# Optimization experiments

Hardware: AMD Instinct MI355X
Metric: run time of the kernel (lower is better)

## Reference

```python
import jax, jax.numpy as jnp
import numpy as np

R, TR = 47, 2  # response_size, treat_size


def _lstm_cell(x, h, c, Wih, Whh, bih, bhh):
    # PyTorch gate order: i, f, g, o
    gates = x @ Wih.T + h @ Whh.T + bih + bhh
    i, f, g, o = jnp.split(gates, 4, axis=-1)
    c_new = jax.nn.sigmoid(f) * c + jax.nn.sigmoid(i) * jnp.tanh(g)
    h_new = jax.nn.sigmoid(o) * jnp.tanh(c_new)
    return h_new, c_new


def setup_inputs() -> dict:
    key = jax.random.key(0)
    B, T = 256, 2048
    ks = jax.random.split(key, 20)

    def u(k, shape, H):
        s = 1.0 / np.sqrt(H).astype(np.float32)
        return jax.random.uniform(k, shape, jnp.float32, -s, s)

    return {
        "x_r": jax.random.normal(ks[0], (B, T, R), jnp.float32),
        "x_t": jax.random.normal(ks[1], (B, T, TR), jnp.float32),
        # r_rnn: 2-layer LSTM, input 49 -> hidden 47
        "r_Wih0": u(ks[2], (4 * R, R + TR), R), "r_Whh0": u(ks[3], (4 * R, R), R),
        "r_bih0": u(ks[4], (4 * R,), R), "r_bhh0": u(ks[5], (4 * R,), R),
        "r_Wih1": u(ks[6], (4 * R, R), R), "r_Whh1": u(ks[7], (4 * R, R), R),
        "r_bih1": u(ks[8], (4 * R,), R), "r_bhh1": u(ks[9], (4 * R,), R),
        # t_rnn: 2-layer LSTM, input 96 -> hidden 2
        "t_Wih0": u(ks[10], (4 * TR, 2 * R + TR), TR), "t_Whh0": u(ks[11], (4 * TR, TR), TR),
        "t_bih0": u(ks[12], (4 * TR,), TR), "t_bhh0": u(ks[13], (4 * TR,), TR),
        "t_Wih1": u(ks[14], (4 * TR, TR), TR), "t_Whh1": u(ks[15], (4 * TR, TR), TR),
        "t_bih1": u(ks[16], (4 * TR,), TR), "t_bhh1": u(ks[17], (4 * TR,), TR),
    }


def reference(x_r, x_t,
              r_Wih0, r_Whh0, r_bih0, r_bhh0, r_Wih1, r_Whh1, r_bih1, r_bhh1,
              t_Wih0, t_Whh0, t_bih0, t_bhh0, t_Wih1, t_Whh1, t_bih1, t_bhh1):
    B = x_r.shape[0]
    zR = jnp.zeros((B, R), x_r.dtype)
    zT = jnp.zeros((B, TR), x_r.dtype)

    def step(carry, xs):
        hr0, cr0, hr1, cr1, ht0, ct0, ht1, ct1 = carry
        r, t = xs  # [B,47], [B,2]
        r_in = jnp.concatenate([r, t], axis=-1)              # [B,49]
        hr0, cr0 = _lstm_cell(r_in, hr0, cr0, r_Wih0, r_Whh0, r_bih0, r_bhh0)
        hr1, cr1 = _lstm_cell(hr0, hr1, cr1, r_Wih1, r_Whh1, r_bih1, r_bhh1)
        t_in = jnp.concatenate([r_in, hr1], axis=-1)         # [B,96]
        ht0, ct0 = _lstm_cell(t_in, ht0, ct0, t_Wih0, t_Whh0, t_bih0, t_bhh0)
        ht1, ct1 = _lstm_cell(ht0, ht1, ct1, t_Wih1, t_Whh1, t_bih1, t_bhh1)
        return (hr0, cr0, hr1, cr1, ht0, ct0, ht1, ct1), (hr1, ht1)

    init = (zR, zR, zR, zR, zT, zT, zT, zT)
    xs = (x_r.transpose(1, 0, 2), x_t.transpose(1, 0, 2))    # time-major
    _, (r_seq, t_seq) = jax.lax.scan(step, init, xs)         # [T,B,47], [T,B,2]
    return (r_seq.transpose(1, 0, 2), t_seq.transpose(1, 0, 2))
```

## Files before the change

kernel.cpp:

```cpp
#include <hip/hip_runtime.h>

#define T_STEPS 2048
#define TOTAL   2080

typedef float f2 __attribute__((ext_vector_type(2)));

__device__ __forceinline__ float fast_rcp(float x) { return __builtin_amdgcn_rcpf(x); }

__device__ __forceinline__ float sig_f(float x) {
    return fast_rcp(1.0f + __expf(-x));
}
__device__ __forceinline__ float tanh_f(float x) {
    float e = __expf(-2.0f * x);
    return fmaf(2.0f, fast_rcp(1.0f + e), -1.0f);
}
__device__ __forceinline__ float gate_act(float x, float zm, float sm, float sa) {
    float e = __expf(-x * zm);
    return fmaf(fast_rcp(1.0f + e), sm, sa);
}

#define LDS_BARRIER() asm volatile("s_waitcnt lgkmcnt(0)\n\ts_barrier" ::: "memory")

#define DPP_BCAST0 0x00
#define DPP_BCAST1 0x55
#define DPP_BCAST2 0xAA
#define DPP_BCAST3 0xFF
#define DPP_ROR4   0x124
#define DPP_ROR8   0x128
template<int CTRL>
__device__ __forceinline__ float dppf(float x) {
    int r = __builtin_amdgcn_update_dpp(0, __builtin_bit_cast(int, x), CTRL, 0xF, 0xF, true);
    return __builtin_bit_cast(float, r);
}

__device__ __forceinline__ void loadx4(float (&dst)[4], const float* __restrict__ x_r,
                                       const float* __restrict__ x_t,
                                       size_t xrb, size_t xtb, int l) {
#pragma unroll
    for (int u = 0; u < 4; ++u) {
        int v = l + 16 * u;
        dst[u] = (v < 47) ? x_r[xrb + v] : ((v < 49) ? x_t[xtb + (v - 47)] : 0.0f);
    }
}

__device__ __forceinline__ void unpack12(f2 (&in)[24], const float4* __restrict__ r4) {
#pragma unroll
    for (int u = 0; u < 12; ++u) {
        float4 v = r4[u];
        in[2 * u]     = f2{v.x, v.y};
        in[2 * u + 1] = f2{v.z, v.w};
    }
}

__device__ __forceinline__ void dot4(float (&pre)[4], const f2 (&in)[24],
                                     const f2 (&w)[4][24], float4 init) {
    f2 a0 = f2{init.x, 0.f}, a1 = f2{init.y, 0.f}, a2 = f2{init.z, 0.f}, a3 = f2{init.w, 0.f};
#pragma unroll
    for (int u = 0; u < 24; ++u) {
        a0 = __builtin_elementwise_fma(w[0][u], in[u], a0);
        a1 = __builtin_elementwise_fma(w[1][u], in[u], a1);
        a2 = __builtin_elementwise_fma(w[2][u], in[u], a2);
        a3 = __builtin_elementwise_fma(w[3][u], in[u], a3);
    }
    pre[0] = a0.x + a0.y; pre[1] = a1.x + a1.y;
    pre[2] = a2.x + a2.y; pre[3] = a3.x + a3.y;
}

__global__ __launch_bounds__(320, 1) void adrnn_fused(
    const float* __restrict__ x_r, const float* __restrict__ x_t,
    const float* __restrict__ rWih0, const float* __restrict__ rWhh0,
    const float* __restrict__ rbih0, const float* __restrict__ rbhh0,
    const float* __restrict__ rWih1, const float* __restrict__ rWhh1,
    const float* __restrict__ rbih1, const float* __restrict__ rbhh1,
    const float* __restrict__ tWih0, const float* __restrict__ tWhh0,
    const float* __restrict__ tbih0, const float* __restrict__ tbhh0,
    const float* __restrict__ tWih1, const float* __restrict__ tWhh1,
    const float* __restrict__ tbih1, const float* __restrict__ tbhh1,
    float* __restrict__ r_out, float* __restrict__ t_out)
{
    __shared__ __align__(16) float tring[64][112];
    __shared__ __align__(16) float h0ring[16][48];
    __shared__ __align__(16) float pAring[16][188];
    __shared__ __align__(16) float pBring[16][188];

    const int tid = threadIdx.x;
    const int wid = tid >> 6;
    const int l   = tid & 63;
    const int j   = l;
    const int b = blockIdx.x;
    const size_t xr_base = (size_t)b * T_STEPS * 47;
    const size_t xt_base = (size_t)b * T_STEPS * 2;

    if (tid < 256) {
        for (int k = tid; k < 64 * 48; k += 256) tring[k / 48][64 + (k % 48)] = 0.0f;
        for (int k = tid; k < 16 * 48; k += 256) h0ring[k / 48][k % 48] = 0.0f;
    }

    if (wid == 0) {
        f2 w[4][24]; float w48[4]; float4 bias = {0, 0, 0, 0};
#pragma unroll
        for (int g = 0; g < 4; ++g) { w48[g] = 0.f;
#pragma unroll
            for (int u = 0; u < 24; ++u) w[g][u] = f2{0.f, 0.f}; }
        if (j < 47) {
            float bb[4];
#pragma unroll
            for (int g = 0; g < 4; ++g) {
                const int row = g * 47 + j;
#pragma unroll
                for (int u = 0; u < 24; ++u)
                    w[g][u] = f2{rWih0[row * 49 + 2 * u], rWih0[row * 49 + 2 * u + 1]};
                w48[g] = rWih0[row * 49 + 48];
                bb[g] = rbih0[row] + rbhh0[row];
            }
            bias = {bb[0], bb[1], bb[2], bb[3]};
        }
        __syncthreads();
        for (int i = 0; i < TOTAL; ++i) {
            if (i < T_STEPS && j < 47) {
                f2 in[24];
                unpack12(in, (const float4*)&tring[i & 63][0]);
                float x48 = tring[i & 63][48];
                float pre[4];
                dot4(pre, in, w, bias);
                float4 out;
                out.x = fmaf(w48[0], x48, pre[0]);
                out.y = fmaf(w48[1], x48, pre[1]);
                out.z = fmaf(w48[2], x48, pre[2]);
                out.w = fmaf(w48[3], x48, pre[3]);
                *(float4*)&pAring[i & 15][j * 4] = out;
            }
            if ((i & 7) == 7) LDS_BARRIER();
        }
    } else if (wid == 1) {
        f2 w[4][24];
#pragma unroll
        for (int g = 0; g < 4; ++g)
#pragma unroll
            for (int u = 0; u < 24; ++u) w[g][u] = f2{0.f, 0.f};
        if (j < 47) {
#pragma unroll
            for (int g = 0; g < 4; ++g) {
                const int row = g * 47 + j;
#pragma unroll
                for (int u = 0; u < 23; ++u)
                    w[g][u] = f2{rWhh0[row * 47 + 2 * u], rWhh0[row * 47 + 2 * u + 1]};
                w[g][23] = f2{rWhh0[row * 47 + 46], 0.f};
            }
        }
        float c0 = 0.f;
        __syncthreads();
        for (int i = 0; i < TOTAL; ++i) {
            const int s = i - 8;
            if (s >= 0 && s < T_STEPS && j < 47) {
                float4 pa = *(const float4*)&pAring[s & 15][j * 4];
                f2 in[24];
                unpack12(in, (const float4*)&h0ring[(s - 1) & 15][0]);
                float pre[4];
                dot4(pre, in, w, pa);
                float iv = sig_f(pre[0]), fv = sig_f(pre[1]);
                float gv = tanh_f(pre[2]), ov = sig_f(pre[3]);
                c0 = fmaf(fv, c0, iv * gv);
                float h = ov * tanh_f(c0);
                h0ring[s & 15][j] = h;
            }
            if ((i & 7) == 7) LDS_BARRIER();
        }
    } else if (wid == 2) {
        f2 w[4][24]; float4 bias = {0, 0, 0, 0};
#pragma unroll
        for (int g = 0; g < 4; ++g)
#pragma unroll
            for (int u = 0; u < 24; ++u) w[g][u] = f2{0.f, 0.f};
        if (j < 47) {
            float bb[4];
#pragma unroll
            for (int g = 0; g < 4; ++g) {
                const int row = g * 47 + j;
#pragma unroll
                for (int u = 0; u < 23; ++u)
                    w[g][u] = f2{rWih1[row * 47 + 2 * u], rWih1[row * 47 + 2 * u + 1]};
                w[g][23] = f2{rWih1[row * 47 + 46], 0.f};
                bb[g] = rbih1[row] + rbhh1[row];
            }
            bias = {bb[0], bb[1], bb[2], bb[3]};
        }
        __syncthreads();
        for (int i = 0; i < TOTAL; ++i) {
            const int s = i - 16;
            if (s >= 0 && s < T_STEPS && j < 47) {
                f2 in[24];
                unpack12(in, (const float4*)&h0ring[s & 15][0]);
                float pre[4];
                dot4(pre, in, w, bias);
                *(float4*)&pBring[s & 15][j * 4] = float4{pre[0], pre[1], pre[2], pre[3]};
            }
            if ((i & 7) == 7) LDS_BARRIER();
        }
    } else if (wid == 3) {
        f2 w[4][24];
#pragma unroll
        for (int g = 0; g < 4; ++g)
#pragma unroll
            for (int u = 0; u < 24; ++u) w[g][u] = f2{0.f, 0.f};
        if (j < 47) {
#pragma unroll
            for (int g = 0; g < 4; ++g) {
                const int row = g * 47 + j;
#pragma unroll
                for (int u = 0; u < 23; ++u)
                    w[g][u] = f2{rWhh1[row * 47 + 2 * u], rWhh1[row * 47 + 2 * u + 1]};
                w[g][23] = f2{rWhh1[row * 47 + 46], 0.f};
            }
        }
        float c1 = 0.f;
        __syncthreads();
        for (int i = 0; i < TOTAL; ++i) {
            const int s = i - 24;
            if (s >= 0 && s < T_STEPS && j < 47) {
                float4 pb = *(const float4*)&pBring[s & 15][j * 4];
                f2 in[24];
                unpack12(in, (const float4*)&tring[(s - 1) & 63][64]);
                float pre[4];
                dot4(pre, in, w, pb);
                float iv = sig_f(pre[0]), fv = sig_f(pre[1]);
                float gv = tanh_f(pre[2]), ov = sig_f(pre[3]);
                c1 = fmaf(fv, c1, iv * gv);
                float h = ov * tanh_f(c1);
                tring[s & 63][64 + j] = h;
                r_out[((size_t)b * T_STEPS + s) * 47 + j] = h;
            }
            if ((i & 7) == 7) LDS_BARRIER();
        }
    } else {
        const int u  = (l >> 2) & 1;
        const int g  = l & 3;
        const int hf = (l >> 3) & 1;
        const int R0 = g * 2 + u;
        f2 wt[24]; float wx48;
        if (hf == 0) {
            wx48 = 0.f;
#pragma unroll
            for (int k = 0; k < 24; ++k)
                wt[k] = f2{tWih0[R0 * 96 + 2 * k], tWih0[R0 * 96 + 2 * k + 1]};
        } else {
            wx48 = tWih0[R0 * 96 + 48];
#pragma unroll
            for (int k = 0; k < 23; ++k)
                wt[k] = f2{tWih0[R0 * 96 + 49 + 2 * k], tWih0[R0 * 96 + 49 + 2 * k + 1]};
            wt[23] = f2{tWih0[R0 * 96 + 95], 0.f};
        }
        const float bT0 = tbih0[R0] + tbhh0[R0];
        const float wh00 = tWhh0[R0 * 2 + 0], wh01 = tWhh0[R0 * 2 + 1];
        const float wi10 = tWih1[R0 * 2 + 0], wi11 = tWih1[R0 * 2 + 1];
        const float wh10 = tWhh1[R0 * 2 + 0], wh11 = tWhh1[R0 * 2 + 1];
        const float bT1 = tbih1[R0] + tbhh1[R0];
        const bool isg = (g == 2);
        const float zm = isg ? 2.f : 1.f, sm = isg ? 2.f : 1.f, sa = isg ? -1.f : 0.f;
        float ht00 = 0.f, ht01 = 0.f, ct0u = 0.f;
        float ht10 = 0.f, ht11 = 0.f, ct1u = 0.f;

        float xa[4] = {0,0,0,0}, xb[4] = {0,0,0,0}, xc[4] = {0,0,0,0};
        if (l < 16) {
            for (int t = 0; t < 8; ++t) {
                float xv[4];
                loadx4(xv, x_r, x_t, xr_base + (size_t)t * 47, xt_base + (size_t)t * 2, l);
#pragma unroll
                for (int uu = 0; uu < 4; ++uu) {
                    int v = l + 16 * uu;
                    if (v < 49) tring[t][v] = xv[uu];
                }
            }
            loadx4(xa, x_r, x_t, xr_base + (size_t)8 * 47,  xt_base + (size_t)8 * 2,  l);
            loadx4(xb, x_r, x_t, xr_base + (size_t)9 * 47,  xt_base + (size_t)9 * 2,  l);
            loadx4(xc, x_r, x_t, xr_base + (size_t)10 * 47, xt_base + (size_t)10 * 2, l);
        }
        __syncthreads();

        for (int i = 0; i < TOTAL; ++i) {
            if (l < 16) {
                const int tw = i + 8;
                if (tw < T_STEPS) {
#pragma unroll
                    for (int uu = 0; uu < 4; ++uu) {
                        int v = l + 16 * uu;
                        if (v < 49) tring[tw & 63][v] = xa[uu];
                    }
                }
#pragma unroll
                for (int uu = 0; uu < 4; ++uu) { xa[uu] = xb[uu]; xb[uu] = xc[uu]; }
                int tl = i + 11;
                if (tl > T_STEPS - 1) tl = T_STEPS - 1;
                loadx4(xc, x_r, x_t, xr_base + (size_t)tl * 47, xt_base + (size_t)tl * 2, l);
            }
            const int s = i - 32;
            if (s >= 0 && s < T_STEPS) {
                f2 in[24];
                unpack12(in, (const float4*)&tring[s & 63][hf ? 64 : 0]);
                float x48 = tring[s & 63][48];
                f2 av = {0, 0}, bv = {0, 0};
#pragma unroll
                for (int k = 0; k < 12; ++k) {
                    av = __builtin_elementwise_fma(wt[2 * k],     in[2 * k],     av);
                    bv = __builtin_elementwise_fma(wt[2 * k + 1], in[2 * k + 1], bv);
                }
                f2 sv = av + bv;
                float part = fmaf(wx48, x48, sv.x + sv.y);
                float pre0 = part + dppf<DPP_ROR8>(part);
                pre0 += bT0 + wh00 * ht00 + wh01 * ht01;
                float a0 = gate_act(pre0, zm, sm, sa);
                float i0 = dppf<DPP_BCAST0>(a0);
                float f0 = dppf<DPP_BCAST1>(a0);
                float g0 = dppf<DPP_BCAST2>(a0);
                float o0 = dppf<DPP_BCAST3>(a0);
                ct0u = fmaf(f0, ct0u, i0 * g0);
                float htu = o0 * tanh_f(ct0u);
                float hto = dppf<DPP_ROR4>(htu);
                ht00 = (u == 0) ? htu : hto;
                ht01 = (u == 0) ? hto : htu;
                float pre1 = bT1 + wi10 * ht00 + wi11 * ht01 + wh10 * ht10 + wh11 * ht11;
                float a1 = gate_act(pre1, zm, sm, sa);
                float ji = dppf<DPP_BCAST0>(a1);
                float jf = dppf<DPP_BCAST1>(a1);
                float jg = dppf<DPP_BCAST2>(a1);
                float jo = dppf<DPP_BCAST3>(a1);
                ct1u = fmaf(jf, ct1u, ji * jg);
                float h1u = jo * tanh_f(ct1u);
                float h1o = dppf<DPP_ROR4>(h1u);
                ht10 = (u == 0) ? h1u : h1o;
                ht11 = (u == 0) ? h1o : h1u;
                if (l == 0) {
                    float2 tv = {ht10, ht11};
                    *reinterpret_cast<float2*>(&t_out[((size_t)b * T_STEPS + s) * 2]) = tv;
                }
            }
            if ((i & 7) == 7) LDS_BARRIER();
        }
    }
}

extern "C" void kernel_launch(void* const* d_in, const int* in_sizes, int n_in,
                              void* d_out, int out_size, void* d_ws, size_t ws_size,
                              hipStream_t stream) {
    const float* x_r   = (const float*)d_in[0];
    const float* x_t   = (const float*)d_in[1];
    const float* rWih0 = (const float*)d_in[2];
    const float* rWhh0 = (const float*)d_in[3];
    const float* rbih0 = (const float*)d_in[4];
    const float* rbhh0 = (const float*)d_in[5];
    const float* rWih1 = (const float*)d_in[6];
    const float* rWhh1 = (const float*)d_in[7];
    const float* rbih1 = (const float*)d_in[8];
    const float* rbhh1 = (const float*)d_in[9];
    const float* tWih0 = (const float*)d_in[10];
    const float* tWhh0 = (const float*)d_in[11];
    const float* tbih0 = (const float*)d_in[12];
    const float* tbhh0 = (const float*)d_in[13];
    const float* tWih1 = (const float*)d_in[14];
    const float* tWhh1 = (const float*)d_in[15];
    const float* tbih1 = (const float*)d_in[16];
    const float* tbhh1 = (const float*)d_in[17];

    float* r_out = (float*)d_out;
    float* t_out = r_out + (size_t)256 * T_STEPS * 47;

    hipLaunchKernelGGL(adrnn_fused, dim3(256), dim3(320), 0, stream,
                       x_r, x_t, rWih0, rWhh0, rbih0, rbhh0, rWih1, rWhh1, rbih1, rbhh1,
                       tWih0, tWhh0, tbih0, tbhh0, tWih1, tWhh1, tbih1, tbhh1,
                       r_out, t_out);
}
```

Measured before the change: 1.443 ms.

## Use fp16 packed dot products for recurrent LSTM matvecs with fp16 hidden rings

```diff
diff --git a/kernel.cpp b/kernel.cpp
--- a/kernel.cpp
+++ b/kernel.cpp
@@ -4,6 +4,7 @@
 #define TOTAL   2080
 
 typedef float f2 __attribute__((ext_vector_type(2)));
+typedef _Float16 h2 __attribute__((ext_vector_type(2)));
 
 __device__ __forceinline__ float fast_rcp(float x) { return __builtin_amdgcn_rcpf(x); }
 
@@ -18,6 +19,14 @@
     float e = __expf(-x * zm);
     return fmaf(fast_rcp(1.0f + e), sm, sa);
 }
+
+#if __has_builtin(__builtin_amdgcn_fdot2)
+#define FDOT2(a, b, c) __builtin_amdgcn_fdot2((a), (b), (c), false)
+#else
+__device__ __forceinline__ float FDOT2(h2 a, h2 b, float c) {
+    return fmaf((float)a.x, (float)b.x, fmaf((float)a.y, (float)b.y, c));
+}
+#endif
 
 #define LDS_BARRIER() asm volatile("s_waitcnt lgkmcnt(0)\n\ts_barrier" ::: "memory")
 
@@ -25,6 +34,7 @@
 #define DPP_BCAST1 0x55
 #define DPP_BCAST2 0xAA
 #define DPP_BCAST3 0xFF
+#define DPP_PAIR   0xF5
 #define DPP_ROR4   0x124
 #define DPP_ROR8   0x128
 template<int CTRL>
@@ -52,21 +62,38 @@
     }
 }
 
-__device__ __forceinline__ void dot4(float (&pre)[4], const f2 (&in)[24],
-                                     const f2 (&w)[4][24], float4 init) {
-    f2 a0 = f2{init.x, 0.f}, a1 = f2{init.y, 0.f}, a2 = f2{init.z, 0.f}, a3 = f2{init.w, 0.f};
+__device__ __forceinline__ void unpackh(h2 (&in)[24], const h2* __restrict__ row) {
+    const float4* q = (const float4*)row;
+#pragma unroll
+    for (int k = 0; k < 6; ++k) {
+        float4 v = q[k];
+        in[4 * k + 0] = __builtin_bit_cast(h2, v.x);
+        in[4 * k + 1] = __builtin_bit_cast(h2, v.y);
+        in[4 * k + 2] = __builtin_bit_cast(h2, v.z);
+        in[4 * k + 3] = __builtin_bit_cast(h2, v.w);
+    }
+}
+
+__device__ __forceinline__ float4 dot4h(const h2 (&in)[24], const h2 (&w)[4][24], float4 init) {
+    float a0 = init.x, a1 = init.y, a2 = init.z, a3 = init.w;
 #pragma unroll
     for (int u = 0; u < 24; ++u) {
-        a0 = __builtin_elementwise_fma(w[0][u], in[u], a0);
-        a1 = __builtin_elementwise_fma(w[1][u], in[u], a1);
-        a2 = __builtin_elementwise_fma(w[2][u], in[u], a2);
-        a3 = __builtin_elementwise_fma(w[3][u], in[u], a3);
-    }
-    pre[0] = a0.x + a0.y; pre[1] = a1.x + a1.y;
-    pre[2] = a2.x + a2.y; pre[3] = a3.x + a3.y;
-}
-
-__global__ __launch_bounds__(320, 1) void adrnn_fused(
+        a0 = FDOT2(w[0][u], in[u], a0);
+        a1 = FDOT2(w[1][u], in[u], a1);
+        a2 = FDOT2(w[2][u], in[u], a2);
+        a3 = FDOT2(w[3][u], in[u], a3);
+    }
+    return float4{a0, a1, a2, a3};
+}
+
+__device__ __forceinline__ void loadw47h(h2 (&w)[24], const float* __restrict__ src) {
+#pragma unroll
+    for (int u = 0; u < 23; ++u)
+        w[u] = h2{(_Float16)src[2 * u], (_Float16)src[2 * u + 1]};
+    w[23] = h2{(_Float16)src[46], (_Float16)0.0f};
+}
+
+__global__ __launch_bounds__(320) void adrnn_fused(
     const float* __restrict__ x_r, const float* __restrict__ x_t,
     const float* __restrict__ rWih0, const float* __restrict__ rWhh0,
     const float* __restrict__ rbih0, const float* __restrict__ rbhh0,
@@ -79,9 +106,10 @@
     float* __restrict__ r_out, float* __restrict__ t_out)
 {
     __shared__ __align__(16) float tring[64][112];
-    __shared__ __align__(16) float h0ring[16][48];
-    __shared__ __align__(16) float pAring[16][188];
-    __shared__ __align__(16) float pBring[16][188];
+    __shared__ __align__(16) h2 h0f16[16][32];
+    __shared__ __align__(16) h2 h1f16[16][32];
+    __shared__ __align__(16) float pAring[16][192];
+    __shared__ __align__(16) float pBring[16][192];
 
     const int tid = threadIdx.x;
     const int wid = tid >> 6;
@@ -93,7 +121,10 @@
 
     if (tid < 256) {
         for (int k = tid; k < 64 * 48; k += 256) tring[k / 48][64 + (k % 48)] = 0.0f;
-        for (int k = tid; k < 16 * 48; k += 256) h0ring[k / 48][k % 48] = 0.0f;
+        for (int k = tid; k < 16 * 32; k += 256) {
+            h0f16[k >> 5][k & 31] = h2{(_Float16)0.0f, (_Float16)0.0f};
+            h1f16[k >> 5][k & 31] = h2{(_Float16)0.0f, (_Float16)0.0f};
+        }
     }
 
     if (wid == 0) {
@@ -115,120 +146,120 @@
             }
             bias = {bb[0], bb[1], bb[2], bb[3]};
         }
+        const int jsw4 = (j ^ (j >> 3)) * 4;
         __syncthreads();
         for (int i = 0; i < TOTAL; ++i) {
             if (i < T_STEPS && j < 47) {
                 f2 in[24];
                 unpack12(in, (const float4*)&tring[i & 63][0]);
                 float x48 = tring[i & 63][48];
-                float pre[4];
-                dot4(pre, in, w, bias);
+                f2 a0 = f2{bias.x, 0.f}, a1 = f2{bias.y, 0.f}, a2 = f2{bias.z, 0.f}, a3 = f2{bias.w, 0.f};
+#pragma unroll
+                for (int u = 0; u < 24; ++u) {
+                    a0 = __builtin_elementwise_fma(w[0][u], in[u], a0);
+                    a1 = __builtin_elementwise_fma(w[1][u], in[u], a1);
+                    a2 = __builtin_elementwise_fma(w[2][u], in[u], a2);
+                    a3 = __builtin_elementwise_fma(w[3][u], in[u], a3);
+                }
                 float4 out;
-                out.x = fmaf(w48[0], x48, pre[0]);
-                out.y = fmaf(w48[1], x48, pre[1]);
-                out.z = fmaf(w48[2], x48, pre[2]);
-                out.w = fmaf(w48[3], x48, pre[3]);
-                *(float4*)&pAring[i & 15][j * 4] = out;
+                out.x = fmaf(w48[0], x48, a0.x + a0.y);
+                out.y = fmaf(w48[1], x48, a1.x + a1.y);
+                out.z = fmaf(w48[2], x48, a2.x + a2.y);
+                out.w = fmaf(w48[3], x48, a3.x + a3.y);
+                *(float4*)&pAring[i & 15][jsw4] = out;
             }
             if ((i & 7) == 7) LDS_BARRIER();
         }
     } else if (wid == 1) {
-        f2 w[4][24];
+        h2 w[4][24];
 #pragma unroll
         for (int g = 0; g < 4; ++g)
 #pragma unroll
-            for (int u = 0; u < 24; ++u) w[g][u] = f2{0.f, 0.f};
+            for (int u = 0; u < 24; ++u) w[g][u] = h2{(_Float16)0.0f, (_Float16)0.0f};
         if (j < 47) {
 #pragma unroll
-            for (int g = 0; g < 4; ++g) {
-                const int row = g * 47 + j;
-#pragma unroll
-                for (int u = 0; u < 23; ++u)
-                    w[g][u] = f2{rWhh0[row * 47 + 2 * u], rWhh0[row * 47 + 2 * u + 1]};
-                w[g][23] = f2{rWhh0[row * 47 + 46], 0.f};
-            }
-        }
+            for (int g = 0; g < 4; ++g) loadw47h(w[g], &rWhh0[(g * 47 + j) * 47]);
+        }
+        const int jsw4 = (j ^ (j >> 3)) * 4;
         float c0 = 0.f;
         __syncthreads();
         for (int i = 0; i < TOTAL; ++i) {
             const int s = i - 8;
+            float hv = 0.0f;
             if (s >= 0 && s < T_STEPS && j < 47) {
-                float4 pa = *(const float4*)&pAring[s & 15][j * 4];
-                f2 in[24];
-                unpack12(in, (const float4*)&h0ring[(s - 1) & 15][0]);
-                float pre[4];
-                dot4(pre, in, w, pa);
-                float iv = sig_f(pre[0]), fv = sig_f(pre[1]);
-                float gv = tanh_f(pre[2]), ov = sig_f(pre[3]);
+                float4 pa = *(const float4*)&pAring[s & 15][jsw4];
+                h2 in[24];
+                unpackh(in, &h0f16[(s - 1) & 15][0]);
+                float4 pre = dot4h(in, w, pa);
+                float iv = sig_f(pre.x), fv = sig_f(pre.y);
+                float gv = tanh_f(pre.z), ov = sig_f(pre.w);
                 c0 = fmaf(fv, c0, iv * gv);
-                float h = ov * tanh_f(c0);
-                h0ring[s & 15][j] = h;
+                hv = ov * tanh_f(c0);
+            }
+            float hn = dppf<DPP_PAIR>(hv);
+            if (s >= 0 && s < T_STEPS && j < 47 && !(j & 1)) {
+                h0f16[s & 15][j >> 1] = __builtin_bit_cast(h2, __builtin_amdgcn_cvt_pkrtz(hv, hn));
             }
             if ((i & 7) == 7) LDS_BARRIER();
         }
     } else if (wid == 2) {
-        f2 w[4][24]; float4 bias = {0, 0, 0, 0};
+        h2 w[4][24]; float4 bias = {0, 0, 0, 0};
 #pragma unroll
         for (int g = 0; g < 4; ++g)
 #pragma unroll
-            for (int u = 0; u < 24; ++u) w[g][u] = f2{0.f, 0.f};
+            for (int u = 0; u < 24; ++u) w[g][u] = h2{(_Float16)0.0f, (_Float16)0.0f};
         if (j < 47) {
             float bb[4];
 #pragma unroll
             for (int g = 0; g < 4; ++g) {
-                const int row = g * 47 + j;
-#pragma unroll
-                for (int u = 0; u < 23; ++u)
-                    w[g][u] = f2{rWih1[row * 47 + 2 * u], rWih1[row * 47 + 2 * u + 1]};
-                w[g][23] = f2{rWih1[row * 47 + 46], 0.f};
-                bb[g] = rbih1[row] + rbhh1[row];
+                loadw47h(w[g], &rWih1[(g * 47 + j) * 47]);
+                bb[g] = rbih1[g * 47 + j] + rbhh1[g * 47 + j];
             }
             bias = {bb[0], bb[1], bb[2], bb[3]};
         }
+        const int jsw4 = (j ^ (j >> 3)) * 4;
         __syncthreads();
         for (int i = 0; i < TOTAL; ++i) {
             const int s = i - 16;
             if (s >= 0 && s < T_STEPS && j < 47) {
-                f2 in[24];
-                unpack12(in, (const float4*)&h0ring[s & 15][0]);
-                float pre[4];
-                dot4(pre, in, w, bias);
-                *(float4*)&pBring[s & 15][j * 4] = float4{pre[0], pre[1], pre[2], pre[3]};
+                h2 in[24];
+                unpackh(in, &h0f16[s & 15][0]);
+                float4 pre = dot4h(in, w, bias);
+                *(float4*)&pBring[s & 15][jsw4] = pre;
             }
             if ((i & 7) == 7) LDS_BARRIER();
         }
     } else if (wid == 3) {
-        f2 w[4][24];
+        h2 w[4][24];
 #pragma unroll
         for (int g = 0; g < 4; ++g)
 #pragma unroll
-            for (int u = 0; u < 24; ++u) w[g][u] = f2{0.f, 0.f};
+            for (int u = 0; u < 24; ++u) w[g][u] = h2{(_Float16)0.0f, (_Float16)0.0f};
         if (j < 47) {
 #pragma unroll
-            for (int g = 0; g < 4; ++g) {
-                const int row = g * 47 + j;
-#pragma unroll
-                for (int u = 0; u < 23; ++u)
-                    w[g][u] = f2{rWhh1[row * 47 + 2 * u], rWhh1[row * 47 + 2 * u + 1]};
-                w[g][23] = f2{rWhh1[row * 47 + 46], 0.f};
-            }
-        }
+            for (int g = 0; g < 4; ++g) loadw47h(w[g], &rWhh1[(g * 47 + j) * 47]);
+        }
+        const int jsw4 = (j ^ (j >> 3)) * 4;
         float c1 = 0.f;
         __syncthreads();
         for (int i = 0; i < TOTAL; ++i) {
             const int s = i - 24;
+            float hv = 0.0f;
             if (s >= 0 && s < T_STEPS && j < 47) {
-                float4 pb = *(const float4*)&pBring[s & 15][j * 4];
-                f2 in[24];
-                unpack12(in, (const float4*)&tring[(s - 1) & 63][64]);
-                float pre[4];
-                dot4(pre, in, w, pb);
-                float iv = sig_f(pre[0]), fv = sig_f(pre[1]);
-                float gv = tanh_f(pre[2]), ov = sig_f(pre[3]);
+                float4 pb = *(const float4*)&pBring[s & 15][jsw4];
+                h2 in[24];
+                unpackh(in, &h1f16[(s - 1) & 15][0]);
+                float4 pre = dot4h(in, w, pb);
+                float iv = sig_f(pre.x), fv = sig_f(pre.y);
+                float gv = tanh_f(pre.z), ov = sig_f(pre.w);
                 c1 = fmaf(fv, c1, iv * gv);
-                float h = ov * tanh_f(c1);
-                tring[s & 63][64 + j] = h;
-                r_out[((size_t)b * T_STEPS + s) * 47 + j] = h;
+                hv = ov * tanh_f(c1);
+                tring[s & 63][64 + j] = hv;
+                r_out[((size_t)b * T_STEPS + s) * 47 + j] = hv;
+            }
+            float hn = dppf<DPP_PAIR>(hv);
+            if (s >= 0 && s < T_STEPS && j < 47 && !(j & 1)) {
+                h1f16[s & 15][j >> 1] = __builtin_bit_cast(h2, __builtin_amdgcn_cvt_pkrtz(hv, hn));
             }
             if ((i & 7) == 7) LDS_BARRIER();
         }
```

Result: no change. 1.445 ms (+0.1%).
